# Kernel optimization log

Hardware: AMD Instinct MI355X
Metric: run time of the kernel (lower is better)

Reference implementation:

```python
import jax, jax.numpy as jnp
import numpy as np


def _prelu(v, a):
    return jnp.where(v >= 0, v, a * v)


def setup_inputs() -> dict:
    key = jax.random.key(0)
    B, H, L, N, DC = 16, 64, 16384, 32, 128
    ks = jax.random.split(key, 10)
    x = jax.random.normal(ks[0], (B, H, L), jnp.float32)
    cond = jax.random.normal(ks[1], (B, DC), jnp.float32)
    # input pointwise linear (applied over channel dim)
    linear_w = jax.random.normal(ks[2], (H, H), jnp.float32) / np.sqrt(H)
    linear_b = jnp.zeros((H,), jnp.float32)
    prelu1_a = jnp.float32(0.25)
    # S4D parameters (S4D-Lin init): A = -exp(log_A_real) + i*A_imag
    log_dt = jax.random.uniform(ks[3], (H,), jnp.float32,
                                minval=float(np.log(1e-3)), maxval=float(np.log(1e-1)))
    log_A_real = jnp.log(0.5 * jnp.ones((H, N), jnp.float32))
    A_imag = jnp.tile(np.pi * jnp.arange(N, dtype=np.float32), (H, 1))
    C_re = 0.5 * jax.random.normal(ks[4], (H, N), jnp.float32)
    C_im = 0.5 * jax.random.normal(ks[5], (H, N), jnp.float32)
    Dskip = jax.random.normal(ks[6], (H,), jnp.float32)
    # S4 output position-wise linear
    out_w = jax.random.normal(ks[7], (H, H), jnp.float32) / np.sqrt(H)
    out_b = jnp.zeros((H,), jnp.float32)
    # FiLM: cond -> (gamma, beta)
    film_w = jax.random.normal(ks[8], (2 * H, DC), jnp.float32) / np.sqrt(DC)
    film_b = jnp.zeros((2 * H,), jnp.float32)
    prelu2_a = jnp.float32(0.25)
    # depthwise 1x1 conv residual: one scalar per channel
    res_w = jax.random.normal(ks[9], (H,), jnp.float32) / np.sqrt(H)
    return dict(x=x, cond=cond, linear_w=linear_w, linear_b=linear_b,
                prelu1_a=prelu1_a, log_dt=log_dt, log_A_real=log_A_real,
                A_imag=A_imag, C_re=C_re, C_im=C_im, Dskip=Dskip,
                out_w=out_w, out_b=out_b, film_w=film_w, film_b=film_b,
                prelu2_a=prelu2_a, res_w=res_w)


def reference(x, cond, linear_w, linear_b, prelu1_a, log_dt, log_A_real,
              A_imag, C_re, C_im, Dskip, out_w, out_b, film_w, film_b,
              prelu2_a, res_w):
    B, H, L = x.shape
    # linear over channel dim (B H L -> B L H -> linear -> B H L)
    h = jnp.einsum('gh,bhl->bgl', linear_w, x) + linear_b[None, :, None]
    h = _prelu(h, prelu1_a)
    # ---- S4D kernel generation (ZOH discretization) ----
    dt = jnp.exp(log_dt)                       # (H,)
    A = -jnp.exp(log_A_real) + 1j * A_imag     # (H, N) complex
    dtA = A * dt[:, None]                      # (H, N)
    Cd = (C_re + 1j * C_im) * (jnp.exp(dtA) - 1.0) / A
    vand = jnp.exp(dtA[:, :, None] * jnp.arange(L, dtype=jnp.float32))  # (H,N,L)
    K = 2.0 * jnp.einsum('hn,hnl->hl', Cd, vand).real  # (H, L)
    # ---- FFT convolution (causal, linear conv via 2L-point FFT) ----
    n = 2 * L
    y = jnp.fft.irfft(jnp.fft.rfft(h, n=n) * jnp.fft.rfft(K, n=n), n=n)[..., :L]
    y = y + h * Dskip[None, :, None]
    # S4 output position-wise linear
    y = jnp.einsum('gh,bhl->bgl', out_w, y) + out_b[None, :, None]
    # BatchNorm1d(affine=False), training-mode batch statistics
    mean = jnp.mean(y, axis=(0, 2), keepdims=True)
    var = jnp.var(y, axis=(0, 2), keepdims=True)
    y = (y - mean) / jnp.sqrt(var + 1e-5)
    # FiLM conditioning
    gb = cond @ film_w.T + film_b              # (B, 2H)
    gamma, beta = jnp.split(gb, 2, axis=-1)
    y = gamma[:, :, None] * y + beta[:, :, None]
    y = _prelu(y, prelu2_a)
    # depthwise 1x1 conv residual
    return y + res_w[None, :, None] * x
```

## Files before the change

kernel.cpp:

```cpp
#include <hip/hip_runtime.h>
#include <math.h>

#define BB 16
#define HH 64
#define LL 16384
#define NST 32
#define LC 256
#define CC 64
#define BL (BB*LL)

typedef _Float16 f16;
typedef f16  f16x8 __attribute__((ext_vector_type(8)));
typedef float f32x4 __attribute__((ext_vector_type(4)));

#define OFF_H   ((size_t)0)
#define OFF_P   ((size_t)8388608)
#define OFF_S   ((size_t)12582912)
#define OFF_T   ((size_t)14680064)
#define OFF_V   ((size_t)16777216)
#define OFF_U   ((size_t)17301504)
#define OFF_PW  ((size_t)17825792)
#define OFF_WL  ((size_t)17833984)
#define OFF_GB  ((size_t)17838080)
#define OFF_BN  ((size_t)17840128)
#define OFF_BNF ((size_t)17840256)

__global__ void k0_setup(const float* __restrict__ log_dt,
                         const float* __restrict__ log_A_real,
                         const float* __restrict__ A_imag,
                         const float* __restrict__ C_re,
                         const float* __restrict__ C_im,
                         const float* __restrict__ cond,
                         const float* __restrict__ film_w,
                         const float* __restrict__ film_b,
                         float* __restrict__ ws) {
    int t = threadIdx.x, bid = blockIdx.x;
    if (bid < 8) {
        float4* pw = (float4*)(ws + OFF_PW);
        float2* wl = (float2*)(ws + OFF_WL);
        int idx = bid * 256 + t;
        int ch = idx >> 5;
        float dt  = expf(log_dt[ch]);
        float are = -expf(log_A_real[idx]);
        float aim = A_imag[idx];
        float dr = are * dt, di = aim * dt;
        float er = expf(dr);
        float wr = er * cosf(di);
        float wi = er * sinf(di);
        float inv = 1.0f / (are * are + aim * aim);
        float gr = ((wr - 1.0f) * are + wi * aim) * inv;
        float gi = (wi * are - (wr - 1.0f) * aim) * inv;
        float cr = C_re[idx], ci = C_im[idx];
        float cdr = cr * gr - ci * gi;
        float cdi = cr * gi + ci * gr;
        pw[idx] = make_float4(wr, wi, 2.0f * cdr, 2.0f * cdi);
        float erL = expf(dr * (float)LC);
        wl[idx] = make_float2(erL * cosf(di * (float)LC), erL * sinf(di * (float)LC));
    } else {
        float* gb = ws + OFF_GB;
        int o = (bid - 8) * 256 + t;
        int b = o >> 7, j = o & 127;
        float acc = film_b[j];
        for (int q = 0; q < 128; q++)
            acc = fmaf(cond[b * 128 + q], film_w[j * 128 + q], acc);
        gb[o] = acc;
        if (bid == 8 && t < 128) ws[OFF_BN + t] = 0.0f;
    }
}

__global__ __launch_bounds__(256) void kbuild(const float* __restrict__ log_dt,
                                              const float* __restrict__ log_A,
                                              const float* __restrict__ A_imag,
                                              const float* __restrict__ Dskip,
                                              float* __restrict__ ws) {
    __shared__ float Kl[256];
    __shared__ float drs[32], dis[32], c2r[32], c2i[32];
    int bid = blockIdx.x;
    int ch = bid >> 3, part = bid & 7;
    int t = threadIdx.x;
    if (t < 32) {
        float dt = expf(log_dt[ch]);
        float are = -expf(log_A[ch * 32 + t]);
        float aim = A_imag[ch * 32 + t];
        drs[t] = are * dt; dis[t] = aim * dt;
        float4 p = ((const float4*)(ws + OFF_PW))[ch * 32 + t];
        c2r[t] = p.z; c2i[t] = p.w;
    }
    __syncthreads();
    float acc = 0.0f;
    float fd = (float)t;
    for (int n = 0; n < 32; n++) {
        float e = expf(drs[n] * fd);
        float ph = dis[n] * fd;
        acc += c2r[n] * e * cosf(ph) - c2i[n] * e * sinf(ph);
    }
    if (t == 0) acc += Dskip[ch];
    Kl[t] = acc;
    __syncthreads();
    f16* T = (f16*)(ws + OFF_T) + (size_t)ch * 65536;
    {
        int r0 = part * 32;
#pragma unroll
        for (int i = 0; i < 4; i++) {
            int idx = t + i * 256;
            int row = r0 + (idx >> 5);
            int c0 = (idx & 31) * 8;
            f16 vals[8];
#pragma unroll
            for (int j = 0; j < 8; j++) {
                int c = c0 + j;
                vals[j] = (f16)((c <= row) ? Kl[row - c] : 0.0f);
            }
            *(float4*)(T + (size_t)row * 256 + c0) = *(const float4*)vals;
        }
    }
    if (part < 4) {
        f16* V = (f16*)(ws + OFF_V) + (size_t)ch * 16384;
#pragma unroll
        for (int i = 0; i < 2; i++) {
            int idx = t + i * 256;
            int row = part * 16 + (idx >> 5);
            int c0 = (idx & 31) * 8;
            int n = row & 31;
            f16 vals[8];
#pragma unroll
            for (int j = 0; j < 8; j++) {
                float fe = (float)(255 - (c0 + j));
                float e = expf(drs[n] * fe);
                float ph = dis[n] * fe;
                vals[j] = (f16)((row < 32) ? e * cosf(ph) : e * sinf(ph));
            }
            *(float4*)(V + (size_t)row * 256 + c0) = *(const float4*)vals;
        }
    } else {
        f16* U = (f16*)(ws + OFF_U) + (size_t)ch * 16384;
#pragma unroll
        for (int i = 0; i < 2; i++) {
            int idx = t + i * 256;
            int l = (part - 4) * 64 + (idx >> 3);
            int c0 = (idx & 7) * 8;
            float fl1 = (float)(l + 1);
            f16 vals[8];
#pragma unroll
            for (int j = 0; j < 8; j++) {
                int col = c0 + j;
                int n = col >> 1, ri = col & 1;
                float e = expf(drs[n] * fl1);
                float ph = dis[n] * fl1;
                float wre = e * cosf(ph), wim = e * sinf(ph);
                float re = c2r[n] * wre - c2i[n] * wim;
                float im = c2r[n] * wim + c2i[n] * wre;
                vals[j] = (f16)(ri ? -im : re);
            }
            *(float4*)(U + (size_t)l * 64 + c0) = *(const float4*)vals;
        }
    }
}

__global__ __launch_bounds__(256) void k_cm1m(const float* __restrict__ x,
                                              const float* __restrict__ W,
                                              const float* __restrict__ bias,
                                              f16* __restrict__ dst,
                                              const float* __restrict__ aptr) {
    int t = threadIdx.x, bi = blockIdx.x;
    int b = bi >> 6;
    int wv = t >> 6, lane = t & 63;
    int qd = lane >> 4, ln = lane & 15;
    int colw = ((bi & 63) << 8) + wv * 64;
    const float* xb = x + (size_t)b * HH * LL;
    f32x4 acc[4][4];
#pragma unroll
    for (int a = 0; a < 4; a++)
#pragma unroll
        for (int nb = 0; nb < 4; nb++) acc[a][nb] = (f32x4)0.0f;
#pragma unroll
    for (int ks = 0; ks < 2; ks++) {
        f16x8 whi[4], wlo[4];
#pragma unroll
        for (int a = 0; a < 4; a++) {
            const float* wp = W + (size_t)(a * 16 + ln) * 64 + ks * 32 + qd * 8;
#pragma unroll
            for (int j = 0; j < 8; j++) {
                float f = wp[j];
                f16 hv = (f16)f;
                whi[a][j] = hv;
                wlo[a][j] = (f16)(f - (float)hv);
            }
        }
        f16x8 bhi[4], blo[4];
#pragma unroll
        for (int nb = 0; nb < 4; nb++) {
            const float* xp = xb + (size_t)(ks * 32 + qd * 8) * LL + colw + nb * 16 + ln;
#pragma unroll
            for (int j = 0; j < 8; j++) {
                float f = xp[(size_t)j * LL];
                f16 hv = (f16)f;
                bhi[nb][j] = hv;
                blo[nb][j] = (f16)(f - (float)hv);
            }
        }
#pragma unroll
        for (int a = 0; a < 4; a++)
#pragma unroll
            for (int nb = 0; nb < 4; nb++)
                acc[a][nb] = __builtin_amdgcn_mfma_f32_16x16x32_f16(whi[a], bhi[nb], acc[a][nb], 0, 0, 0);
#pragma unroll
        for (int a = 0; a < 4; a++)
#pragma unroll
            for (int nb = 0; nb < 4; nb++)
                acc[a][nb] = __builtin_amdgcn_mfma_f32_16x16x32_f16(whi[a], blo[nb], acc[a][nb], 0, 0, 0);
#pragma unroll
        for (int a = 0; a < 4; a++)
#pragma unroll
            for (int nb = 0; nb < 4; nb++)
                acc[a][nb] = __builtin_amdgcn_mfma_f32_16x16x32_f16(wlo[a], bhi[nb], acc[a][nb], 0, 0, 0);
    }
    float a1 = *aptr;
    f16* dp = dst + (size_t)b * HH * LL;
#pragma unroll
    for (int a = 0; a < 4; a++)
#pragma unroll
        for (int r = 0; r < 4; r++) {
            int g = a * 16 + qd * 4 + r;
            float bb = bias[g];
            f16* gp = dp + (size_t)g * LL + colw + ln;
#pragma unroll
            for (int nb = 0; nb < 4; nb++) {
                float v = acc[a][nb][r] + bb;
                v = (v >= 0.0f) ? v : a1 * v;
                gp[nb * 16] = (f16)v;
            }
        }
}

__global__ __launch_bounds__(256) void k_cm2m(const f16* __restrict__ y1,
                                              const float* __restrict__ W,
                                              const float* __restrict__ bias,
                                              float* __restrict__ dst) {
    int t = threadIdx.x, bi = blockIdx.x;
    int b = bi >> 6;
    int wv = t >> 6, lane = t & 63;
    int qd = lane >> 4, ln = lane & 15;
    int colw = ((bi & 63) << 8) + wv * 64;
    const f16* yb = y1 + (size_t)b * HH * LL;
    f32x4 acc[4][4];
#pragma unroll
    for (int a = 0; a < 4; a++)
#pragma unroll
        for (int nb = 0; nb < 4; nb++) acc[a][nb] = (f32x4)0.0f;
#pragma unroll
    for (int ks = 0; ks < 2; ks++) {
        f16x8 whi[4], wlo[4];
#pragma unroll
        for (int a = 0; a < 4; a++) {
            const float* wp = W + (size_t)(a * 16 + ln) * 64 + ks * 32 + qd * 8;
#pragma unroll
            for (int j = 0; j < 8; j++) {
                float f = wp[j];
                f16 hv = (f16)f;
                whi[a][j] = hv;
                wlo[a][j] = (f16)(f - (float)hv);
            }
        }
        f16x8 bf[4];
#pragma unroll
        for (int nb = 0; nb < 4; nb++) {
            const f16* yp = yb + (size_t)(ks * 32 + qd * 8) * LL + colw + nb * 16 + ln;
#pragma unroll
            for (int j = 0; j < 8; j++)
                bf[nb][j] = yp[(size_t)j * LL];
        }
#pragma unroll
        for (int a = 0; a < 4; a++)
#pragma unroll
            for (int nb = 0; nb < 4; nb++)
                acc[a][nb] = __builtin_amdgcn_mfma_f32_16x16x32_f16(whi[a], bf[nb], acc[a][nb], 0, 0, 0);
#pragma unroll
        for (int a = 0; a < 4; a++)
#pragma unroll
            for (int nb = 0; nb < 4; nb++)
                acc[a][nb] = __builtin_amdgcn_mfma_f32_16x16x32_f16(wlo[a], bf[nb], acc[a][nb], 0, 0, 0);
    }
    float* dp = dst + (size_t)b * HH * LL;
#pragma unroll
    for (int a = 0; a < 4; a++)
#pragma unroll
        for (int r = 0; r < 4; r++) {
            int g = a * 16 + qd * 4 + r;
            float bb = bias[g];
            float* gp = dp + (size_t)g * LL + colw + ln;
#pragma unroll
            for (int nb = 0; nb < 4; nb++)
                gp[nb * 16] = acc[a][nb][r] + bb;
        }
}

__global__ __launch_bounds__(256) void gemmA(float* __restrict__ ws) {
    __shared__ __align__(16) char smem[25600];
    f16* Vs = (f16*)smem;
    f16* Hs = (f16*)(smem + 5120);
    int t = threadIdx.x;
    int bid = blockIdx.x;
    int ch = bid & 63, ntile = bid >> 6;
    const f16* Vm = (const f16*)(ws + OFF_V) + (size_t)ch * 16384;
    const f16* H  = (const f16*)(ws + OFF_H);
    int w = t >> 6, lane = t & 63;
    int qd = lane >> 4, ln = lane & 15;
    f32x4 acc[4][4];
#pragma unroll
    for (int a = 0; a < 4; a++)
#pragma unroll
        for (int nb = 0; nb < 4; nb++) acc[a][nb] = (f32x4)0.0f;
    int colg = ntile * 256 + t;
    const f16* hcol = H + ((size_t)(colg >> 6) * 64 + ch) * 16384 + (size_t)(colg & 63) * 256;
    int vrow = t >> 2, vkg = t & 3;
    for (int k0 = 0; k0 < 256; k0 += 32) {
        __syncthreads();
        *(float4*)&Vs[vrow * 40 + vkg * 8] = *(const float4*)(Vm + vrow * 256 + k0 + vkg * 8);
#pragma unroll
        for (int kg = 0; kg < 4; kg++)
            *(float4*)&Hs[t * 40 + kg * 8] = *(const float4*)(hcol + k0 + kg * 8);
        __syncthreads();
        f16x8 af[4], bf[4];
#pragma unroll
        for (int a = 0; a < 4; a++) af[a] = *(f16x8*)&Vs[(a * 16 + ln) * 40 + qd * 8];
#pragma unroll
        for (int nb = 0; nb < 4; nb++) bf[nb] = *(f16x8*)&Hs[(w * 64 + nb * 16 + ln) * 40 + qd * 8];
#pragma unroll
        for (int a = 0; a < 4; a++)
#pragma unroll
            for (int nb = 0; nb < 4; nb++)
                acc[a][nb] = __builtin_amdgcn_mfma_f32_16x16x32_f16(af[a], bf[nb], acc[a][nb], 0, 0, 0);
    }
    float* P = ws + OFF_P;
#pragma unroll
    for (int a = 0; a < 4; a++)
#pragma unroll
        for (int nb = 0; nb < 4; nb++)
#pragma unroll
            for (int r = 0; r < 4; r++) {
                int row = a * 16 + qd * 4 + r;
                int col = ntile * 256 + w * 64 + nb * 16 + ln;
                P[((size_t)ch * 64 + row) * 1024 + col] = acc[a][nb][r];
            }
}

__global__ __launch_bounds__(256) void k3_scan(float* __restrict__ ws) {
    int tid = blockIdx.x * 256 + threadIdx.x;
    int ch = tid >> 9, b = (tid >> 5) & 15, n = tid & 31;
    const float* P = ws + OFF_P;
    f16* S = (f16*)(ws + OFF_S);
    float2 wl = ((const float2*)(ws + OFF_WL))[ch * 32 + n];
    float sr = 0.0f, si = 0.0f;
    const float* pre = P + ((size_t)ch * 64 + n) * 1024 + b * 64;
    const float* pim = P + ((size_t)ch * 64 + 32 + n) * 1024 + b * 64;
    f16* srow = S + ((size_t)ch * 1024 + b * 64) * 64 + 2 * n;
    for (int c = 0; c < 64; c++) {
        srow[c * 64]     = (f16)sr;
        srow[c * 64 + 1] = (f16)si;
        float pr = pre[c], pi = pim[c];
        float nr = fmaf(wl.x, sr, fmaf(-wl.y, si, pr));
        float ni = fmaf(wl.y, sr, fmaf(wl.x, si, pi));
        sr = nr; si = ni;
    }
}

__global__ __launch_bounds__(256) void gemmMain(float* __restrict__ ws) {
    __shared__ __align__(16) char smem[25600];
    f16* Ts = (f16*)smem;
    f16* Hs = (f16*)(smem + 20480);
    f16* Ys = (f16*)smem;
    int t = threadIdx.x;
    int bid = blockIdx.x;
    int ch = bid & 63, ntile = bid >> 6;
    const f16* Tm = (const f16*)(ws + OFF_T) + (size_t)ch * 65536;
    const f16* Um = (const f16*)(ws + OFF_U) + (size_t)ch * 16384;
    const f16* H  = (const f16*)(ws + OFF_H);
    const f16* St = (const f16*)(ws + OFF_S);
    f16* y1 = (f16*)(ws + OFF_H);
    int w = t >> 6, lane = t & 63;
    int qd = lane >> 4, ln = lane & 15;
    f32x4 acc[4][4];
#pragma unroll
    for (int a = 0; a < 4; a++)
#pragma unroll
        for (int nb = 0; nb < 4; nb++) acc[a][nb] = (f32x4)0.0f;
    int scol = t >> 2, skg = t & 3;
    int colg = ntile * 64 + scol;
    const f16* hcol = H + ((size_t)(colg >> 6) * 64 + ch) * 16384 + (size_t)(colg & 63) * 256;
    const f16* sscol = St + ((size_t)ch * 1024 + colg) * 64;
    for (int k0 = 0; k0 < 256; k0 += 32) {
        __syncthreads();
#pragma unroll
        for (int kg = 0; kg < 4; kg++)
            *(float4*)&Ts[t * 40 + kg * 8] = *(const float4*)(Tm + t * 256 + k0 + kg * 8);
        *(float4*)&Hs[scol * 40 + skg * 8] = *(const float4*)(hcol + k0 + skg * 8);
        __syncthreads();
        if (k0 <= w * 64 + 63) {
            f16x8 bf[4];
#pragma unroll
            for (int nb = 0; nb < 4; nb++) bf[nb] = *(f16x8*)&Hs[(nb * 16 + ln) * 40 + qd * 8];
#pragma unroll
            for (int a = 0; a < 4; a++) {
                if (k0 <= w * 64 + a * 16 + 15) {
                    f16x8 af = *(f16x8*)&Ts[(w * 64 + a * 16 + ln) * 40 + qd * 8];
#pragma unroll
                    for (int nb = 0; nb < 4; nb++)
                        acc[a][nb] = __builtin_amdgcn_mfma_f32_16x16x32_f16(af, bf[nb], acc[a][nb], 0, 0, 0);
                }
            }
        }
    }
    for (int k0 = 0; k0 < 64; k0 += 32) {
        __syncthreads();
#pragma unroll
        for (int kg = 0; kg < 4; kg++)
            *(float4*)&Ts[t * 40 + kg * 8] = *(const float4*)(Um + t * 64 + k0 + kg * 8);
        *(float4*)&Hs[scol * 40 + skg * 8] = *(const float4*)(sscol + k0 + skg * 8);
        __syncthreads();
        f16x8 bf[4];
#pragma unroll
        for (int nb = 0; nb < 4; nb++) bf[nb] = *(f16x8*)&Hs[(nb * 16 + ln) * 40 + qd * 8];
#pragma unroll
        for (int a = 0; a < 4; a++) {
            f16x8 af = *(f16x8*)&Ts[(w * 64 + a * 16 + ln) * 40 + qd * 8];
#pragma unroll
            for (int nb = 0; nb < 4; nb++)
                acc[a][nb] = __builtin_amdgcn_mfma_f32_16x16x32_f16(af, bf[nb], acc[a][nb], 0, 0, 0);
        }
    }
    int ocol = t >> 2, ojg = t & 3;
    int ocolg = ntile * 64 + ocol;
    f16* ybase = y1 + ((size_t)(ocolg >> 6) * 64 + ch) * 16384 + (size_t)(ocolg & 63) * 256;
    for (int hf = 0; hf < 2; hf++) {
        __syncthreads();
        if ((w >> 1) == hf) {
            int jl0 = (w & 1) * 64;
#pragma unroll
            for (int a = 0; a < 4; a++)
#pragma unroll
                for (int nb = 0; nb < 4; nb++)
#pragma unroll
                    for (int r = 0; r < 4; r++)
                        Ys[(nb * 16 + ln) * 136 + jl0 + a * 16 + qd * 4 + r] = (f16)acc[a][nb][r];
        }
        __syncthreads();
#pragma unroll
        for (int i = 0; i < 4; i++)
            *(float4*)(ybase + hf * 128 + ojg * 32 + i * 8) =
                *(const float4*)&Ys[ocol * 136 + ojg * 32 + i * 8];
    }
}

__global__ __launch_bounds__(256) void k5b_bnsum(const float* __restrict__ y2,
                                                 float* __restrict__ ws) {
    int bi = blockIdx.x;
    int t = threadIdx.x;
    const float4* r4 = (const float4*)(y2 + (size_t)bi * LL);
    float s = 0.0f, ss = 0.0f;
    for (int i = 0; i < 16; i++) {
        float4 v = r4[t + i * 256];
        s += v.x + v.y + v.z + v.w;
        ss += v.x * v.x + v.y * v.y + v.z * v.z + v.w * v.w;
    }
    for (int off = 32; off; off >>= 1) {
        s += __shfl_xor(s, off);
        ss += __shfl_xor(ss, off);
    }
    __shared__ float wsum[4], wsq[4];
    int wv = t >> 6;
    if ((t & 63) == 0) { wsum[wv] = s; wsq[wv] = ss; }
    __syncthreads();
    if (t == 0) {
        float S = wsum[0] + wsum[1] + wsum[2] + wsum[3];
        float SS = wsq[0] + wsq[1] + wsq[2] + wsq[3];
        int ch = bi & 63;
        atomicAdd(ws + OFF_BN + ch, S);
        atomicAdd(ws + OFF_BN + 64 + ch, SS);
    }
}

__global__ void k5c_bnfin(float* __restrict__ ws) {
    int t = threadIdx.x;
    float cnt = (float)BL;
    float mean = ws[OFF_BN + t] / cnt;
    float var = ws[OFF_BN + 64 + t] / cnt - mean * mean;
    ws[OFF_BNF + t] = mean;
    ws[OFF_BNF + 64 + t] = 1.0f / sqrtf(var + 1e-5f);
}

__global__ __launch_bounds__(256) void k6_final(const float* __restrict__ x,
                                                const float* __restrict__ ws,
                                                const float* __restrict__ a2p,
                                                const float* __restrict__ res_w,
                                                float* __restrict__ out) {
    int bi = blockIdx.x;
    int t = threadIdx.x;
    int row = bi >> 4;
    int b = row >> 6, ch = row & 63;
    float gamma = ws[OFF_GB + b * 128 + ch];
    float beta  = ws[OFF_GB + b * 128 + 64 + ch];
    float mean = ws[OFF_BNF + ch];
    float inv  = ws[OFF_BNF + 64 + ch];
    float scale = gamma * inv;
    float shift = beta - scale * mean;
    float rw = res_w[ch];
    float a2 = *a2p;
    size_t i4 = (size_t)row * (LL / 4) + (size_t)(bi & 15) * 256 + t;
    float4 y = ((const float4*)out)[i4];
    float4 xv = ((const float4*)x)[i4];
    float v;
    v = fmaf(scale, y.x, shift); v = (v >= 0.0f) ? v : a2 * v; y.x = fmaf(rw, xv.x, v);
    v = fmaf(scale, y.y, shift); v = (v >= 0.0f) ? v : a2 * v; y.y = fmaf(rw, xv.y, v);
    v = fmaf(scale, y.z, shift); v = (v >= 0.0f) ? v : a2 * v; y.z = fmaf(rw, xv.z, v);
    v = fmaf(scale, y.w, shift); v = (v >= 0.0f) ? v : a2 * v; y.w = fmaf(rw, xv.w, v);
    ((float4*)out)[i4] = y;
}

extern "C" void kernel_launch(void* const* d_in, const int* in_sizes, int n_in,
                              void* d_out, int out_size, void* d_ws, size_t ws_size,
                              hipStream_t stream) {
    const float* x        = (const float*)d_in[0];
    const float* cond     = (const float*)d_in[1];
    const float* linear_w = (const float*)d_in[2];
    const float* linear_b = (const float*)d_in[3];
    const float* prelu1_a = (const float*)d_in[4];
    const float* log_dt   = (const float*)d_in[5];
    const float* log_A    = (const float*)d_in[6];
    const float* A_imag   = (const float*)d_in[7];
    const float* C_re     = (const float*)d_in[8];
    const float* C_im     = (const float*)d_in[9];
    const float* Dskip    = (const float*)d_in[10];
    const float* out_w    = (const float*)d_in[11];
    const float* out_b    = (const float*)d_in[12];
    const float* film_w   = (const float*)d_in[13];
    const float* film_b   = (const float*)d_in[14];
    const float* prelu2_a = (const float*)d_in[15];
    const float* res_w    = (const float*)d_in[16];
    float* ws  = (float*)d_ws;
    float* out = (float*)d_out;
    f16* hbuf = (f16*)(ws + OFF_H);
    f16* y1   = (f16*)(ws + OFF_H);

    hipLaunchKernelGGL(k0_setup, dim3(16), dim3(256), 0, stream,
                       log_dt, log_A, A_imag, C_re, C_im, cond, film_w, film_b, ws);
    hipLaunchKernelGGL(kbuild, dim3(512), dim3(256), 0, stream,
                       log_dt, log_A, A_imag, Dskip, ws);
    hipLaunchKernelGGL(k_cm1m, dim3(1024), dim3(256), 0, stream,
                       x, linear_w, linear_b, hbuf, prelu1_a);
    hipLaunchKernelGGL(gemmA, dim3(256), dim3(256), 0, stream, ws);
    hipLaunchKernelGGL(k3_scan, dim3(128), dim3(256), 0, stream, ws);
    hipLaunchKernelGGL(gemmMain, dim3(1024), dim3(256), 0, stream, ws);
    hipLaunchKernelGGL(k_cm2m, dim3(1024), dim3(256), 0, stream,
                       y1, out_w, out_b, out);
    hipLaunchKernelGGL(k5b_bnsum, dim3(1024), dim3(256), 0, stream, out, ws);
    hipLaunchKernelGGL(k5c_bnfin, dim3(1), dim3(64), 0, stream, ws);
    hipLaunchKernelGGL(k6_final, dim3(16384), dim3(256), 0, stream,
                       x, ws, prelu2_a, res_w, out);
}
```

Measured before the change: 295.3 us.

## Fuse BatchNorm statistics into output GEMM and load gemmMain operands directly

The BN sum and sum-of-squares are now computed in the epilogue of the output pointwise GEMM. Each block writes its per-channel partials to workspace, and a 64-block finalize kernel reduces them, so the separate full pass that re-read the fp32 output is gone. gemmMain also drops its LDS staging of the T and H tiles and reads MFMA operands straight from global memory, which removes barriers at the cost of uncoalesced, repeated global loads. The atomic zeroing of the BN accumulators is removed because partials are now written deterministically.

```diff
diff --git a/kernel.cpp b/kernel.cpp
--- a/kernel.cpp
+++ b/kernel.cpp
@@ -64,7 +64,6 @@
         for (int q = 0; q < 128; q++)
             acc = fmaf(cond[b * 128 + q], film_w[j * 128 + q], acc);
         gb[o] = acc;
-        if (bid == 8 && t < 128) ws[OFF_BN + t] = 0.0f;
     }
 }
 
@@ -236,13 +235,17 @@
 __global__ __launch_bounds__(256) void k_cm2m(const f16* __restrict__ y1,
                                               const float* __restrict__ W,
                                               const float* __restrict__ bias,
-                                              float* __restrict__ dst) {
+                                              float* __restrict__ dst,
+                                              float* __restrict__ ws) {
+    __shared__ float bns[64], bnss[64];
     int t = threadIdx.x, bi = blockIdx.x;
     int b = bi >> 6;
     int wv = t >> 6, lane = t & 63;
     int qd = lane >> 4, ln = lane & 15;
     int colw = ((bi & 63) << 8) + wv * 64;
     const f16* yb = y1 + (size_t)b * HH * LL;
+    if (t < 64) { bns[t] = 0.0f; bnss[t] = 0.0f; }
+    __syncthreads();
     f32x4 acc[4][4];
 #pragma unroll
     for (int a = 0; a < 4; a++)
@@ -289,10 +292,29 @@
             int g = a * 16 + qd * 4 + r;
             float bb = bias[g];
             float* gp = dp + (size_t)g * LL + colw + ln;
-#pragma unroll
-            for (int nb = 0; nb < 4; nb++)
-                gp[nb * 16] = acc[a][nb][r] + bb;
-        }
+            float s = 0.0f, ssq = 0.0f;
+#pragma unroll
+            for (int nb = 0; nb < 4; nb++) {
+                float v = acc[a][nb][r] + bb;
+                gp[nb * 16] = v;
+                s += v; ssq += v * v;
+            }
+#pragma unroll
+            for (int off = 1; off < 16; off <<= 1) {
+                s += __shfl_xor(s, off);
+                ssq += __shfl_xor(ssq, off);
+            }
+            if (ln == 0) {
+                atomicAdd(&bns[g], s);
+                atomicAdd(&bnss[g], ssq);
+            }
+        }
+    __syncthreads();
+    if (t < 64) {
+        float* part = ws + OFF_P;
+        part[(size_t)bi * 128 + t] = bns[t];
+        part[(size_t)bi * 128 + 64 + t] = bnss[t];
+    }
 }
 
 __global__ __launch_bounds__(256) void gemmA(float* __restrict__ ws) {
@@ -366,10 +388,7 @@
 }
 
 __global__ __launch_bounds__(256) void gemmMain(float* __restrict__ ws) {
-    __shared__ __align__(16) char smem[25600];
-    f16* Ts = (f16*)smem;
-    f16* Hs = (f16*)(smem + 20480);
-    f16* Ys = (f16*)smem;
+    __shared__ __align__(16) f16 Ys[64 * 136];
     int t = threadIdx.x;
     int bid = blockIdx.x;
     int ch = bid & 63, ntile = bid >> 6;
@@ -380,30 +399,30 @@
     f16* y1 = (f16*)(ws + OFF_H);
     int w = t >> 6, lane = t & 63;
     int qd = lane >> 4, ln = lane & 15;
+    int rowbase = w * 64;
     f32x4 acc[4][4];
 #pragma unroll
     for (int a = 0; a < 4; a++)
 #pragma unroll
         for (int nb = 0; nb < 4; nb++) acc[a][nb] = (f32x4)0.0f;
-    int scol = t >> 2, skg = t & 3;
-    int colg = ntile * 64 + scol;
-    const f16* hcol = H + ((size_t)(colg >> 6) * 64 + ch) * 16384 + (size_t)(colg & 63) * 256;
-    const f16* sscol = St + ((size_t)ch * 1024 + colg) * 64;
+    const f16* hcolp[4];
+    const f16* scolp[4];
+#pragma unroll
+    for (int nb = 0; nb < 4; nb++) {
+        int colg = ntile * 64 + nb * 16 + ln;
+        hcolp[nb] = H + ((size_t)(colg >> 6) * 64 + ch) * 16384 + (size_t)(colg & 63) * 256;
+        scolp[nb] = St + ((size_t)ch * 1024 + colg) * 64;
+    }
     for (int k0 = 0; k0 < 256; k0 += 32) {
-        __syncthreads();
-#pragma unroll
-        for (int kg = 0; kg < 4; kg++)
-            *(float4*)&Ts[t * 40 + kg * 8] = *(const float4*)(Tm + t * 256 + k0 + kg * 8);
-        *(float4*)&Hs[scol * 40 + skg * 8] = *(const float4*)(hcol + k0 + skg * 8);
-        __syncthreads();
-        if (k0 <= w * 64 + 63) {
+        if (k0 <= rowbase + 63) {
             f16x8 bf[4];
 #pragma unroll
-            for (int nb = 0; nb < 4; nb++) bf[nb] = *(f16x8*)&Hs[(nb * 16 + ln) * 40 + qd * 8];
+            for (int nb = 0; nb < 4; nb++)
+                bf[nb] = *(const f16x8*)(hcolp[nb] + k0 + qd * 8);
 #pragma unroll
             for (int a = 0; a < 4; a++) {
-                if (k0 <= w * 64 + a * 16 + 15) {
-                    f16x8 af = *(f16x8*)&Ts[(w * 64 + a * 16 + ln) * 40 + qd * 8];
+                if (k0 <= rowbase + a * 16 + 15) {
+                    f16x8 af = *(const f16x8*)(Tm + (size_t)(rowbase + a * 16 + ln) * 256 + k0 + qd * 8);
 #pragma unroll
                     for (int nb = 0; nb < 4; nb++)
                         acc[a][nb] = __builtin_amdgcn_mfma_f32_16x16x32_f16(af, bf[nb], acc[a][nb], 0, 0, 0);
@@ -411,19 +430,15 @@
             }
         }
     }
+#pragma unroll
     for (int k0 = 0; k0 < 64; k0 += 32) {
-        __syncthreads();
-#pragma unroll
-        for (int kg = 0; kg < 4; kg++)
-            *(float4*)&Ts[t * 40 + kg * 8] = *(const float4*)(Um + t * 64 + k0 + kg * 8);
-        *(float4*)&Hs[scol * 40 + skg * 8] = *(const float4*)(sscol + k0 + skg * 8);
-        __syncthreads();
         f16x8 bf[4];
 #pragma unroll
-        for (int nb = 0; nb < 4; nb++) bf[nb] = *(f16x8*)&Hs[(nb * 16 + ln) * 40 + qd * 8];
+        for (int nb = 0; nb < 4; nb++)
+            bf[nb] = *(const f16x8*)(scolp[nb] + k0 + qd * 8);
 #pragma unroll
         for (int a = 0; a < 4; a++) {
-            f16x8 af = *(f16x8*)&Ts[(w * 64 + a * 16 + ln) * 40 + qd * 8];
+            f16x8 af = *(const f16x8*)(Um + (size_t)(rowbase + a * 16 + ln) * 64 + k0 + qd * 8);
 #pragma unroll
             for (int nb = 0; nb < 4; nb++)
                 acc[a][nb] = __builtin_amdgcn_mfma_f32_16x16x32_f16(af, bf[nb], acc[a][nb], 0, 0, 0);
@@ -452,41 +467,34 @@
     }
 }
 
-__global__ __launch_bounds__(256) void k5b_bnsum(const float* __restrict__ y2,
-                                                 float* __restrict__ ws) {
-    int bi = blockIdx.x;
+__global__ __launch_bounds__(256) void k5c_bnfin(float* __restrict__ ws) {
+    int ch = blockIdx.x;
     int t = threadIdx.x;
-    const float4* r4 = (const float4*)(y2 + (size_t)bi * LL);
+    const float* part = ws + OFF_P;
     float s = 0.0f, ss = 0.0f;
-    for (int i = 0; i < 16; i++) {
-        float4 v = r4[t + i * 256];
-        s += v.x + v.y + v.z + v.w;
-        ss += v.x * v.x + v.y * v.y + v.z * v.z + v.w * v.w;
+#pragma unroll
+    for (int i = 0; i < 4; i++) {
+        int pb = t + i * 256;
+        s  += part[(size_t)pb * 128 + ch];
+        ss += part[(size_t)pb * 128 + 64 + ch];
     }
     for (int off = 32; off; off >>= 1) {
         s += __shfl_xor(s, off);
         ss += __shfl_xor(ss, off);
     }
-    __shared__ float wsum[4], wsq[4];
+    __shared__ float as_[4], ass_[4];
     int wv = t >> 6;
-    if ((t & 63) == 0) { wsum[wv] = s; wsq[wv] = ss; }
+    if ((t & 63) == 0) { as_[wv] = s; ass_[wv] = ss; }
     __syncthreads();
     if (t == 0) {
-        float S = wsum[0] + wsum[1] + wsum[2] + wsum[3];
-        float SS = wsq[0] + wsq[1] + wsq[2] + wsq[3];
-        int ch = bi & 63;
-        atomicAdd(ws + OFF_BN + ch, S);
-        atomicAdd(ws + OFF_BN + 64 + ch, SS);
-    }
-}
-
-__global__ void k5c_bnfin(float* __restrict__ ws) {
-    int t = threadIdx.x;
-    float cnt = (float)BL;
-    float mean = ws[OFF_BN + t] / cnt;
-    float var = ws[OFF_BN + 64 + t] / cnt - mean * mean;
-    ws[OFF_BNF + t] = mean;
-    ws[OFF_BNF + 64 + t] = 1.0f / sqrtf(var + 1e-5f);
+        float S = as_[0] + as_[1] + as_[2] + as_[3];
+        float SS = ass_[0] + ass_[1] + ass_[2] + ass_[3];
+        float cnt = (float)BL;
+        float mean = S / cnt;
+        float var = SS / cnt - mean * mean;
+        ws[OFF_BNF + ch] = mean;
+        ws[OFF_BNF + 64 + ch] = 1.0f / sqrtf(var + 1e-5f);
+    }
 }
 
 __global__ __launch_bounds__(256) void k6_final(const float* __restrict__ x,
@@ -552,9 +560,8 @@
     hipLaunchKernelGGL(k3_scan, dim3(128), dim3(256), 0, stream, ws);
     hipLaunchKernelGGL(gemmMain, dim3(1024), dim3(256), 0, stream, ws);
     hipLaunchKernelGGL(k_cm2m, dim3(1024), dim3(256), 0, stream,
-                       y1, out_w, out_b, out);
-    hipLaunchKernelGGL(k5b_bnsum, dim3(1024), dim3(256), 0, stream, out, ws);
-    hipLaunchKernelGGL(k5c_bnfin, dim3(1), dim3(64), 0, stream, ws);
+                       y1, out_w, out_b, out, ws);
+    hipLaunchKernelGGL(k5c_bnfin, dim3(64), dim3(256), 0, stream, ws);
     hipLaunchKernelGGL(k6_final, dim3(16384), dim3(256), 0, stream,
                        x, ws, prelu2_a, res_w, out);
 }
```

Measured after the change: 295.6 us. Within noise of the previous version (+0.1%).
